# Optimization experiments

Measured on AMD Instinct MI355X. Metric: run time of the kernel, lower is better.

## Reference

```python
import jax, jax.numpy as jnp
import numpy as np

VOCAB = 512
EMB = 256
HID = 64
T_HORIZON = 0.05


def setup_inputs() -> dict:
    key = jax.random.key(0)
    ks = jax.random.split(key, 6)
    B, L = 32, 4096
    x = jax.random.randint(ks[0], (B, L), 0, VOCAB, dtype=jnp.int64 if jax.config.jax_enable_x64 else jnp.int32)
    emb_table = jax.random.normal(ks[1], (VOCAB, EMB), dtype=jnp.float32)
    W1 = jax.random.normal(ks[2], (EMB, HID), dtype=jnp.float32) * (1.0 / np.sqrt(EMB))
    b1 = jnp.zeros((HID,), dtype=jnp.float32)
    W2 = jax.random.normal(ks[3], (HID, VOCAB), dtype=jnp.float32) * (1.0 / np.sqrt(HID))
    b2 = jnp.full((VOCAB,), 0.1, dtype=jnp.float32)  # torch: bias.data.fill_(0.1)
    return {"x": x, "emb_table": emb_table, "W1": W1, "b1": b1, "W2": W2, "b2": b2, "steps": 5}


def reference(x, emb_table, W1, b1, W2, b2, steps):
    """Vectorized Gillespie-style Markov jump simulation.

    Equivalent to the torch loop: intensity is computed once per step from the
    current state, then every (b, l) position samples a candidate next state
    from softmax(intensity) with the self-transition zeroed and renormalized
    (== categorical over logits with the current state masked to -inf), and
    accepts it with prob 1 - exp(-rate * dt).
    """
    V = emb_table.shape[0]
    dt = T_HORIZON / steps
    key = jax.random.key(42)
    keys = jax.random.split(key, steps)
    vocab_ids = jnp.arange(V)

    def step(x_t, k):
        # intensity: [B, L, V]
        h = jax.nn.relu(emb_table[x_t] @ W1 + b1)
        intensity = h @ W2 + b2
        # mask self-transition (softmax * (1 - onehot) then renormalize)
        self_mask = x_t[..., None] == vocab_ids  # [B, L, V] bool
        masked_logits = jnp.where(self_mask, -jnp.inf, intensity)
        k1, k2 = jax.random.split(k)
        next_state = jax.random.categorical(k1, masked_logits)  # [B, L]
        rate = jnp.take_along_axis(intensity, next_state[..., None], axis=-1)[..., 0]
        accept_prob = 1.0 - jnp.exp(-rate * dt)
        u = jax.random.uniform(k2, x_t.shape, dtype=rate.dtype)
        x_t = jnp.where(u < accept_prob, next_state.astype(x_t.dtype), x_t)
        return x_t, None

    x_final, _ = jax.lax.scan(step, x, keys)
    return x_final
```

## Files before the change

### kernel.cpp

```cpp
#include <hip/hip_runtime.h>
#include <stdint.h>


#define VOCAB  512
#define EMB    256
#define HID    64
#define NPOS   (32 * 4096)
#define STEPS  5
#define PPW    8
#define CHUNKS (NPOS / PPW)
#define MBLK   (CHUNKS / 2)

__host__ __device__ __forceinline__ void tf2x32(uint32_t k0, uint32_t k1,
                                                uint32_t x0, uint32_t x1,
                                                uint32_t& o0, uint32_t& o1) {
  uint32_t ks2 = k0 ^ k1 ^ 0x1BD11BDAu;
  x0 += k0; x1 += k1;
#define TFR(r) { x0 += x1; x1 = (x1 << (r)) | (x1 >> (32 - (r))); x1 ^= x0; }
  TFR(13) TFR(15) TFR(26) TFR(6)
  x0 += k1;  x1 += ks2 + 1u;
  TFR(17) TFR(29) TFR(16) TFR(24)
  x0 += ks2; x1 += k0 + 2u;
  TFR(13) TFR(15) TFR(26) TFR(6)
  x0 += k0;  x1 += k1 + 3u;
  TFR(17) TFR(29) TFR(16) TFR(24)
  x0 += k1;  x1 += ks2 + 4u;
  TFR(13) TFR(15) TFR(26) TFR(6)
  x0 += ks2; x1 += k0 + 5u;
#undef TFR
  o0 = x0; o1 = x1;
}

struct Keys {
  uint32_t k1a[STEPS], k1b[STEPS];
  uint32_t k2a[STEPS], k2b[STEPS];
};

__global__ __launch_bounds__(512)
void build_table(const float* __restrict__ emb,
                 const float* __restrict__ W1,
                 const float* __restrict__ b1,
                 const float* __restrict__ W2,
                 const float* __restrict__ b2,
                 float* __restrict__ I,
                 float* __restrict__ pthr) {
  const int s   = blockIdx.x;
  const int tid = threadIdx.x;
  __shared__ double part[8][HID];
  __shared__ double hd[HID];
  __shared__ float  redmax[8];

  const int hid = tid & (HID - 1);
  const int kq  = tid >> 6;
  const float* e = emb + s * EMB;
  double acc = 0.0;
#pragma unroll
  for (int ib = 0; ib < 32; ib += 16) {
    float ev[16], wv[16];
#pragma unroll
    for (int i = 0; i < 16; ++i) {
      const int k = kq + 8 * (ib + i);
      ev[i] = e[k];
      wv[i] = W1[k * HID + hid];
    }
#pragma unroll
    for (int i = 0; i < 16; ++i)
      acc += (double)ev[i] * (double)wv[i];
  }
  part[kq][hid] = acc;
  __syncthreads();
  if (kq == 0) {
    const double a = ((part[0][hid] + part[1][hid]) + (part[2][hid] + part[3][hid]))
                   + ((part[4][hid] + part[5][hid]) + (part[6][hid] + part[7][hid]));
    const float m = (float)a + b1[hid];
    hd[hid] = (double)(m > 0.0f ? m : 0.0f);
  }
  __syncthreads();

  double acc2 = 0.0;
#pragma unroll
  for (int kb = 0; kb < HID; kb += 16) {
    float wv[16];
#pragma unroll
    for (int i = 0; i < 16; ++i)
      wv[i] = W2[(kb + i) * VOCAB + tid];
#pragma unroll
    for (int i = 0; i < 16; ++i)
      acc2 += hd[kb + i] * (double)wv[i];
  }
  const float val = (float)acc2 + b2[tid];
  I[s * VOCAB + tid] = val;

  float lmax = val;
  for (int off = 32; off > 0; off >>= 1)
    lmax = fmaxf(lmax, __shfl_xor(lmax, off, 64));
  if ((tid & 63) == 0) redmax[tid >> 6] = lmax;
  __syncthreads();
  if (tid == 0) {
    float m = redmax[0];
#pragma unroll
    for (int i = 1; i < 8; ++i) m = fmaxf(m, redmax[i]);
    const float z = (-m) * 0.01f;
    pthr[s] = 1.0f - (float)exp((double)z);
  }
}

__global__ __launch_bounds__(128)
void markov_kernel(const int* __restrict__ x_in,
                   const float* __restrict__ I,
                   const float* __restrict__ pthr,
                   int* __restrict__ x_out,
                   Keys K) {
  const int lane = threadIdx.x & 63;
  const int wid  = threadIdx.x >> 6;
  const int qp = lane / 5;
  const int qt = lane - qp * 5;
  const float TINYF = 1.17549435e-38f;

  const int b = blockIdx.x;
  const int pair = (b & 7) * (MBLK / 8) + (b >> 3);
  const int base = (pair * 2 + wid) * PPW;

  int scur = (lane < PPW) ? x_in[base + lane] : 0;
  const float pv = (lane < PPW) ? pthr[scur] : 0.0f;

  float u40 = 0.0f;
  if (lane < PPW * STEPS) {
    uint32_t w0, w1;
    tf2x32(K.k2a[qt], K.k2b[qt], 0u, (uint32_t)(base + qp), w0, w1);
    u40 = __uint_as_float((((w0 ^ w1) >> 9) | 0x3f800000u)) - 1.0f;
  }

  const float pq = __shfl(pv, qp, 64);
  const bool cand = (lane < PPW * STEPS) && (u40 < pq);
  unsigned long long mask = __ballot(cand);

  while (mask) {
    const int q = (int)__builtin_ctzll(mask);
    mask &= mask - 1;
    const int p = q / 5;
    const int t = q - p * 5;
    const int s = __builtin_amdgcn_readfirstlane(__shfl(scur, p, 64));

    const float* row = I + s * VOCAB;
    float rv[8];
#pragma unroll
    for (int j = 0; j < 8; ++j)
      rv[j] = row[lane + (j << 6)];

    const uint32_t fbase = ((uint32_t)(base + p) << 9) + (uint32_t)lane;
    uint32_t bits[8];
#pragma unroll
    for (int j = 0; j < 8; ++j) {
      uint32_t w0, w1;
      tf2x32(K.k1a[t], K.k1b[t], 0u, fbase + ((uint32_t)j << 6), w0, w1);
      bits[j] = w0 ^ w1;
    }

    float best = -__builtin_inff();
    float rbest = 0.0f;
    int bidx = 0;
#pragma unroll
    for (int j = 0; j < 8; ++j) {
      float ufv = __uint_as_float((bits[j] >> 9) | 0x3f800000u) - 1.0f;
      if (ufv == 0.0f) ufv = TINYF;
      const float g = -logf(-logf(ufv));
      const int v = lane + (j << 6);
      if (v != s) {
        const float val = rv[j] + g;
        if (val > best) { best = val; bidx = v; rbest = rv[j]; }
      }
    }
    for (int off = 32; off > 0; off >>= 1) {
      const float ob = __shfl_xor(best, off, 64);
      const int   oi = __shfl_xor(bidx, off, 64);
      const float orv = __shfl_xor(rbest, off, 64);
      if (ob > best || (ob == best && oi < bidx)) {
        best = ob; bidx = oi; rbest = orv;
      }
    }
    bidx = __builtin_amdgcn_readfirstlane(bidx);
    const float rate = rbest;
    const float z = (-rate) * 0.01f;
    const float pacc = 1.0f - (float)exp((double)z);
    const float u = __shfl(u40, q, 64);
    if (u < pacc) {
      if (lane == p) scur = bidx;
      const unsigned long long fut =
          (((1ull << (p * 5 + 5)) - 1) & ~((1ull << (q + 1)) - 1));
      const float pnew = pthr[bidx];
      const unsigned long long nb = __ballot(u40 < pnew) & fut;
      mask = (mask & ~fut) | nb;
    }
  }
  if (lane < PPW) x_out[base + lane] = scur;
}

extern "C" void kernel_launch(void* const* d_in, const int* in_sizes, int n_in,
                              void* d_out, int out_size, void* d_ws, size_t ws_size,
                              hipStream_t stream) {
  const int*   x   = (const int*)d_in[0];
  const float* emb = (const float*)d_in[1];
  const float* W1  = (const float*)d_in[2];
  const float* b1  = (const float*)d_in[3];
  const float* W2  = (const float*)d_in[4];
  const float* b2  = (const float*)d_in[5];
  float* I    = (float*)d_ws;
  float* pthr = (float*)d_ws + VOCAB * VOCAB;
  int* out = (int*)d_out;

  Keys K;
  for (int t = 0; t < STEPS; ++t) {
    uint32_t Sa, Sb;
    tf2x32(0u, 42u, 0u, (uint32_t)t, Sa, Sb);
    tf2x32(Sa, Sb, 0u, 0u, K.k1a[t], K.k1b[t]);
    tf2x32(Sa, Sb, 0u, 1u, K.k2a[t], K.k2b[t]);
  }

  build_table<<<VOCAB, 512, 0, stream>>>(emb, W1, b1, W2, b2, I, pthr);
  markov_kernel<<<MBLK, 128, 0, stream>>>(x, I, pthr, out, K);
}
```

Baseline: 110.0 us.

## Compact active positions into per-segment queues before running Markov chains

Splits the simulation into a scan kernel and a chain kernel. The scan kernel writes out positions that can never jump and appends the rest to per-segment work queues using atomics. The chain kernel then gives each remaining position its own wavefront, so lanes are no longer wasted on inactive positions and load is balanced across the GPU. The cost is an extra launch, global atomics and queue traffic.

New measurement: 110.3 us. About the same (+0.3%).

```diff
diff --git a/kernel.cpp b/kernel.cpp
--- a/kernel.cpp
+++ b/kernel.cpp
@@ -9,7 +9,10 @@
 #define STEPS  5
 #define PPW    8
 #define CHUNKS (NPOS / PPW)
-#define MBLK   (CHUNKS / 2)
+#define NSEG   8
+#define SEGPOS (NPOS / NSEG)
+#define SCANB  1024
+#define CHAINB 2048
 
 __host__ __device__ __forceinline__ void tf2x32(uint32_t k0, uint32_t k1,
                                                 uint32_t x0, uint32_t x1,
@@ -43,13 +46,16 @@
                  const float* __restrict__ W2,
                  const float* __restrict__ b2,
                  float* __restrict__ I,
-                 float* __restrict__ pthr) {
+                 float* __restrict__ pthr,
+                 int* __restrict__ gcnt) {
   const int s   = blockIdx.x;
   const int tid = threadIdx.x;
   __shared__ double part[8][HID];
   __shared__ double hd[HID];
   __shared__ float  redmax[8];
 
+  if (s < NSEG && tid == 0) gcnt[s * 64] = 0;
+
   const int hid = tid & (HID - 1);
   const int kq  = tid >> 6;
   const float* e = emb + s * EMB;
@@ -105,95 +111,143 @@
   }
 }
 
-__global__ __launch_bounds__(128)
-void markov_kernel(const int* __restrict__ x_in,
-                   const float* __restrict__ I,
-                   const float* __restrict__ pthr,
-                   int* __restrict__ x_out,
-                   Keys K) {
+__global__ __launch_bounds__(256)
+void scan_kernel(const int* __restrict__ x_in,
+                 const float* __restrict__ pthr,
+                 int* __restrict__ x_out,
+                 int* __restrict__ gcnt,
+                 unsigned short* __restrict__ queue,
+                 Keys K) {
+  __shared__ int lcount;
+  __shared__ int lbase;
+  __shared__ int lpos[128];
+  if (threadIdx.x == 0) lcount = 0;
+  __syncthreads();
+
   const int lane = threadIdx.x & 63;
   const int wid  = threadIdx.x >> 6;
   const int qp = lane / 5;
   const int qt = lane - qp * 5;
+  const int b = blockIdx.x;
+
+#pragma unroll
+  for (int cc = 0; cc < 4; ++cc) {
+    const int chunk = b * 16 + wid * 4 + cc;
+    const int base = chunk * PPW;
+
+    const int scur = (lane < PPW) ? x_in[base + lane] : 0;
+    const float pv = (lane < PPW) ? pthr[scur] : 0.0f;
+
+    float u40 = 0.0f;
+    if (lane < PPW * STEPS) {
+      uint32_t w0, w1;
+      tf2x32(K.k2a[qt], K.k2b[qt], 0u, (uint32_t)(base + qp), w0, w1);
+      u40 = __uint_as_float((((w0 ^ w1) >> 9) | 0x3f800000u)) - 1.0f;
+    }
+    const float pq = __shfl(pv, qp, 64);
+    const unsigned long long mask =
+        __ballot((lane < PPW * STEPS) && (u40 < pq));
+
+    const int sh = (lane < PPW) ? lane * 5 : 0;
+    const bool act = (lane < PPW) && (((mask >> sh) & 0x1Full) != 0ull);
+    if (lane < PPW && !act) x_out[base + lane] = scur;
+    if (lane < PPW && act) {
+      const int o = atomicAdd(&lcount, 1);
+      lpos[o] = base + lane;
+    }
+  }
+  __syncthreads();
+  const int seg = b >> 7;
+  if (threadIdx.x == 0) lbase = atomicAdd(&gcnt[seg * 64], lcount);
+  __syncthreads();
+  const int lb = lbase, lc = lcount;
+  for (int i = threadIdx.x; i < lc; i += 256)
+    queue[seg * SEGPOS + lb + i] = (unsigned short)(lpos[i] - seg * SEGPOS);
+}
+
+__global__ __launch_bounds__(256)
+void chain_kernel(const int* __restrict__ x_in,
+                  const float* __restrict__ I,
+                  const float* __restrict__ pthr,
+                  int* __restrict__ x_out,
+                  const int* __restrict__ gcnt,
+                  const unsigned short* __restrict__ queue,
+                  Keys K) {
+  const int lane = threadIdx.x & 63;
+  const int W = blockIdx.x * 4 + (threadIdx.x >> 6);
+  const int seg = W >> 10;
+  const int cnt = gcnt[seg * 64];
   const float TINYF = 1.17549435e-38f;
 
-  const int b = blockIdx.x;
-  const int pair = (b & 7) * (MBLK / 8) + (b >> 3);
-  const int base = (pair * 2 + wid) * PPW;
-
-  int scur = (lane < PPW) ? x_in[base + lane] : 0;
-  const float pv = (lane < PPW) ? pthr[scur] : 0.0f;
-
-  float u40 = 0.0f;
-  if (lane < PPW * STEPS) {
-    uint32_t w0, w1;
-    tf2x32(K.k2a[qt], K.k2b[qt], 0u, (uint32_t)(base + qp), w0, w1);
-    u40 = __uint_as_float((((w0 ^ w1) >> 9) | 0x3f800000u)) - 1.0f;
-  }
-
-  const float pq = __shfl(pv, qp, 64);
-  const bool cand = (lane < PPW * STEPS) && (u40 < pq);
-  unsigned long long mask = __ballot(cand);
-
-  while (mask) {
-    const int q = (int)__builtin_ctzll(mask);
-    mask &= mask - 1;
-    const int p = q / 5;
-    const int t = q - p * 5;
-    const int s = __builtin_amdgcn_readfirstlane(__shfl(scur, p, 64));
-
-    const float* row = I + s * VOCAB;
-    float rv[8];
-#pragma unroll
-    for (int j = 0; j < 8; ++j)
-      rv[j] = row[lane + (j << 6)];
-
-    const uint32_t fbase = ((uint32_t)(base + p) << 9) + (uint32_t)lane;
-    uint32_t bits[8];
-#pragma unroll
-    for (int j = 0; j < 8; ++j) {
+  for (int i = (W & 1023); i < cnt; i += 1024) {
+    const int pos = seg * SEGPOS + (int)queue[seg * SEGPOS + i];
+
+    int s = x_in[pos];
+    float u5 = 0.0f;
+    if (lane < STEPS) {
       uint32_t w0, w1;
-      tf2x32(K.k1a[t], K.k1b[t], 0u, fbase + ((uint32_t)j << 6), w0, w1);
-      bits[j] = w0 ^ w1;
-    }
-
-    float best = -__builtin_inff();
-    float rbest = 0.0f;
-    int bidx = 0;
-#pragma unroll
-    for (int j = 0; j < 8; ++j) {
-      float ufv = __uint_as_float((bits[j] >> 9) | 0x3f800000u) - 1.0f;
-      if (ufv == 0.0f) ufv = TINYF;
-      const float g = -logf(-logf(ufv));
-      const int v = lane + (j << 6);
-      if (v != s) {
-        const float val = rv[j] + g;
-        if (val > best) { best = val; bidx = v; rbest = rv[j]; }
-      }
-    }
-    for (int off = 32; off > 0; off >>= 1) {
-      const float ob = __shfl_xor(best, off, 64);
-      const int   oi = __shfl_xor(bidx, off, 64);
-      const float orv = __shfl_xor(rbest, off, 64);
-      if (ob > best || (ob == best && oi < bidx)) {
-        best = ob; bidx = oi; rbest = orv;
-      }
-    }
-    bidx = __builtin_amdgcn_readfirstlane(bidx);
-    const float rate = rbest;
-    const float z = (-rate) * 0.01f;
-    const float pacc = 1.0f - (float)exp((double)z);
-    const float u = __shfl(u40, q, 64);
-    if (u < pacc) {
-      if (lane == p) scur = bidx;
-      const unsigned long long fut =
-          (((1ull << (p * 5 + 5)) - 1) & ~((1ull << (q + 1)) - 1));
-      const float pnew = pthr[bidx];
-      const unsigned long long nb = __ballot(u40 < pnew) & fut;
-      mask = (mask & ~fut) | nb;
-    }
-  }
-  if (lane < PPW) x_out[base + lane] = scur;
+      tf2x32(K.k2a[lane], K.k2b[lane], 0u, (uint32_t)pos, w0, w1);
+      u5 = __uint_as_float((((w0 ^ w1) >> 9) | 0x3f800000u)) - 1.0f;
+    }
+    const float pv0 = pthr[s];
+    unsigned mask5 =
+        (unsigned)(__ballot(lane < STEPS && u5 < pv0) & 0x1Full);
+
+    while (mask5) {
+      const int t = __builtin_ctz(mask5);
+      mask5 &= mask5 - 1;
+
+      const float* row = I + s * VOCAB;
+      float rv[8];
+#pragma unroll
+      for (int j = 0; j < 8; ++j)
+        rv[j] = row[lane + (j << 6)];
+
+      const uint32_t fbase = ((uint32_t)pos << 9) + (uint32_t)lane;
+      uint32_t bits[8];
+#pragma unroll
+      for (int j = 0; j < 8; ++j) {
+        uint32_t w0, w1;
+        tf2x32(K.k1a[t], K.k1b[t], 0u, fbase + ((uint32_t)j << 6), w0, w1);
+        bits[j] = w0 ^ w1;
+      }
+
+      float best = -__builtin_inff();
+      float rbest = 0.0f;
+      int bidx = 0;
+#pragma unroll
+      for (int j = 0; j < 8; ++j) {
+        float ufv = __uint_as_float((bits[j] >> 9) | 0x3f800000u) - 1.0f;
+        if (ufv == 0.0f) ufv = TINYF;
+        const float g = -logf(-logf(ufv));
+        const int v = lane + (j << 6);
+        if (v != s) {
+          const float val = rv[j] + g;
+          if (val > best) { best = val; bidx = v; rbest = rv[j]; }
+        }
+      }
+      for (int off = 32; off > 0; off >>= 1) {
+        const float ob = __shfl_xor(best, off, 64);
+        const int   oi = __shfl_xor(bidx, off, 64);
+        const float orv = __shfl_xor(rbest, off, 64);
+        if (ob > best || (ob == best && oi < bidx)) {
+          best = ob; bidx = oi; rbest = orv;
+        }
+      }
+      bidx = __builtin_amdgcn_readfirstlane(bidx);
+      const float rate = rbest;
+      const float z = (-rate) * 0.01f;
+      const float pacc = 1.0f - (float)exp((double)z);
+      const float u = __shfl(u5, t, 64);
+      if (u < pacc) {
+        s = bidx;
+        const float pnew = pthr[bidx];
+        mask5 = ((unsigned)(__ballot(lane < STEPS && u5 < pnew) & 0x1Full))
+                & ~((1u << (t + 1)) - 1u);
+      }
+    }
+    if (lane == 0) x_out[pos] = s;
+  }
 }
 
 extern "C" void kernel_launch(void* const* d_in, const int* in_sizes, int n_in,
@@ -205,8 +259,10 @@
   const float* b1  = (const float*)d_in[3];
   const float* W2  = (const float*)d_in[4];
   const float* b2  = (const float*)d_in[5];
-  float* I    = (float*)d_ws;
-  float* pthr = (float*)d_ws + VOCAB * VOCAB;
+  float* I = (float*)d_ws;
+  float* pthr = (float*)((char*)d_ws + 1048576);
+  int*   gcnt = (int*)((char*)d_ws + 1050624);
+  unsigned short* queue = (unsigned short*)((char*)d_ws + 1052672);
   int* out = (int*)d_out;
 
   Keys K;
@@ -217,6 +273,7 @@
     tf2x32(Sa, Sb, 0u, 1u, K.k2a[t], K.k2b[t]);
   }
 
-  build_table<<<VOCAB, 512, 0, stream>>>(emb, W1, b1, W2, b2, I, pthr);
-  markov_kernel<<<MBLK, 128, 0, stream>>>(x, I, pthr, out, K);
-}
+  build_table<<<VOCAB, 512, 0, stream>>>(emb, W1, b1, W2, b2, I, pthr, gcnt);
+  scan_kernel<<<SCANB, 256, 0, stream>>>(x, pthr, out, gcnt, queue, K);
+  chain_kernel<<<CHAINB, 256, 0, stream>>>(x, I, pthr, out, gcnt, queue, K);
+}
```
